# Optimization experiments

Measured on AMD Instinct MI355X. Metric: run time of the kernel, lower is better.

Reference implementation:

```python
import jax, jax.numpy as jnp
import numpy as np

# model constants (match init_kwargs)
D_EQUI = 64
D_INV = 256
D_INV_COND = 256
D_MSG = 64
N_HEADS = 16
D_FF = 256
D_EDGE_IN = 64
D_EDGE_OUT = 64
D_OUT = D_EQUI + N_HEADS + D_EDGE_OUT  # 144
IN_FEATS = 2 * D_MSG + D_EQUI + D_EDGE_IN  # 256
NEG = -1e9

B, N, NC = 2, 256, 512


def setup_inputs() -> dict:
    key = jax.random.key(0)
    ks = jax.random.split(key, 20)
    s = 0.02
    inp = {
        'equis': jax.random.normal(ks[0], (B, N, 3, D_EQUI), jnp.float32),
        'invs': jax.random.normal(ks[1], (B, N, D_INV), jnp.float32),
        'cond_equis': jax.random.normal(ks[2], (B, NC, 3, D_EQUI), jnp.float32),
        'cond_invs': jax.random.normal(ks[3], (B, NC, D_INV_COND), jnp.float32),
        'edges': jax.random.normal(ks[4], (B, N, NC, D_EDGE_IN), jnp.float32),
        'adj_matrix': jax.random.randint(ks[5], (B, N, NC), 0, 2, jnp.int32),
        # pairwise message params
        'q_w': s * jax.random.normal(ks[6], (D_INV, D_MSG), jnp.float32),
        'q_b': jnp.zeros((D_MSG,), jnp.float32),
        'k_w': s * jax.random.normal(ks[7], (D_INV_COND, D_MSG), jnp.float32),
        'k_b': jnp.zeros((D_MSG,), jnp.float32),
        'w1': s * jax.random.normal(ks[8], (IN_FEATS, D_FF), jnp.float32),
        'b1': jnp.zeros((D_FF,), jnp.float32),
        'w2': s * jax.random.normal(ks[9], (D_FF, D_OUT), jnp.float32),
        'b2': jnp.zeros((D_OUT,), jnp.float32),
        # equi attention params (bias-free linears)
        'equi_in_w': s * jax.random.normal(ks[10], (D_EQUI, D_EQUI), jnp.float32),
        'equi_out_w': s * jax.random.normal(ks[11], (D_EQUI, D_EQUI), jnp.float32),
        # inv attention params
        'inv_in_w': s * jax.random.normal(ks[12], (D_INV_COND, D_INV_COND), jnp.float32),
        'inv_in_b': jnp.zeros((D_INV_COND,), jnp.float32),
        'inv_out_w': s * jax.random.normal(ks[13], (D_INV_COND, D_INV), jnp.float32),
        'inv_out_b': jnp.zeros((D_INV,), jnp.float32),
    }
    return inp


def reference(equis, invs, cond_equis, cond_invs, edges, adj_matrix,
              q_w, q_b, k_w, k_b, w1, b1, w2, b2,
              equi_in_w, equi_out_w, inv_in_w, inv_in_b, inv_out_w, inv_out_b):
    # adjacency -> additive attention mask [B,N,NC]
    mask = jnp.where(adj_matrix > 0, 0.0, NEG).astype(equis.dtype)

    # ---- pairwise messages ----
    # per-channel dot products over the coordinate axis: [B,N,NC,D_EQUI]
    dot = jnp.einsum('bqxd,bkxd->bqkd', equis, cond_equis)
    q_msg = invs @ q_w + q_b            # [B,N,D_MSG]
    k_msg = cond_invs @ k_w + k_b       # [B,NC,D_MSG]
    feats = jnp.concatenate([
        jnp.broadcast_to(q_msg[:, :, None, :], (B, N, NC, D_MSG)),
        jnp.broadcast_to(k_msg[:, None, :, :], (B, N, NC, D_MSG)),
        dot,
        edges,
    ], axis=-1)                          # [B,N,NC,IN_FEATS]
    h = jax.nn.silu(feats @ w1 + b1)
    messages = h @ w2 + b2               # [B,N,NC,D_OUT]

    equi_m = messages[..., :D_EQUI]
    inv_m = messages[..., D_EQUI:D_EQUI + N_HEADS]
    edge_out = messages[..., D_EQUI + N_HEADS:]

    # ---- equivariant attention ----
    proj = jnp.einsum('bkxd,de->bkxe', cond_equis, equi_in_w)  # [B,NC,3,D_EQUI]
    attn_e = jax.nn.softmax(equi_m + mask[..., None], axis=2)   # [B,N,NC,D_EQUI]
    eo = jnp.einsum('bqkd,bkxd->bqxd', attn_e, proj)            # [B,N,3,D_EQUI]
    w_e = jnp.sqrt(jnp.sum(attn_e ** 2, axis=2))                # [B,N,D_EQUI]
    eo = eo * w_e[:, :, None, :]
    equi_out = jnp.einsum('bqxd,de->bqxe', eo, equi_out_w)

    # ---- invariant attention ----
    pf = cond_invs @ inv_in_w + inv_in_b                        # [B,NC,D_INV_COND]
    hf = pf.reshape(B, NC, N_HEADS, D_INV_COND // N_HEADS)      # [B,NC,H,dh]
    attn_i = jax.nn.softmax(inv_m + mask[..., None], axis=2)    # [B,N,NC,H]
    io = jnp.einsum('bqkh,bkhd->bqhd', attn_i, hf)              # [B,N,H,dh]
    w_i = jnp.sqrt(jnp.sum(attn_i ** 2, axis=2))                # [B,N,H]
    io = (io * w_i[..., None]).reshape(B, N, D_INV_COND)
    inv_out = io @ inv_out_w + inv_out_b                        # [B,N,D_INV]

    return equi_out, inv_out, edge_out
```

## Files before the change

kernel.cpp:

```cpp
#include <hip/hip_runtime.h>
#include <hip/hip_bf16.h>

#define DEVINL static __device__ __forceinline__

typedef __attribute__((ext_vector_type(8))) short bf16x8;
typedef __attribute__((ext_vector_type(8))) unsigned short us8;
typedef __attribute__((ext_vector_type(4))) float f32x4;
typedef __attribute__((ext_vector_type(4))) unsigned short us4;

DEVINL float siluf(float x) { return x / (1.0f + __expf(-x)); }
DEVINL unsigned short bfb(float x) { __hip_bfloat16 h = __float2bfloat16(x); return *(unsigned short*)&h; }
DEVINL float b2f(unsigned short u) { return __uint_as_float(((unsigned int)u) << 16); }

__global__ void wfrag_kernel(const float* __restrict__ w1, const float* __restrict__ w2,
                             unsigned short* __restrict__ w1f, unsigned short* __restrict__ w2f) {
  const int g = blockIdx.x, tid = threadIdx.x;
  if (g < 16) {
    #pragma unroll
    for (int e2 = 0; e2 < 16; ++e2) {
      const int flat = tid * 16 + e2;
      const int kk = flat >> 9, rem = flat & 511, ln = rem >> 3, e = rem & 7;
      const int c = g * 16 + (ln & 15);
      const int k = kk * 32 + (ln >> 4) * 8 + e;
      w1f[(size_t)g * 4096 + flat] = bfb(w1[(size_t)k * 256 + c]);
    }
  } else {
    const int t = g - 16;
    #pragma unroll
    for (int e2 = 0; e2 < 16; ++e2) {
      const int flat = tid * 16 + e2;
      const int kk = flat >> 9, rem = flat & 511, ln = rem >> 3, e = rem & 7;
      const int c = t * 16 + (ln & 15);
      const int k = kk * 32 + (ln >> 4) * 8 + e;
      w2f[(size_t)t * 4096 + flat] = bfb(w2[(size_t)k * 144 + c]);
    }
  }
}

__global__ void cet_kernel(const float* __restrict__ ce, unsigned short* __restrict__ cet) {
  const size_t i = (size_t)blockIdx.x * 192 + threadIdx.x;
  cet[i] = bfb(ce[i]);
}

__global__ void qk_kernel(const float* __restrict__ invs, const float* __restrict__ cond_invs,
                          const float* __restrict__ qw, const float* __restrict__ qb,
                          const float* __restrict__ kw, const float* __restrict__ kb2,
                          float* __restrict__ qm, float* __restrict__ km) {
  __shared__ float srow[256];
  const int r = blockIdx.x;
  const float* in; const float* w; const float* bias; float* out; int row;
  if (r < 512) { in = invs;      w = qw; bias = qb;  out = qm; row = r; }
  else         { in = cond_invs; w = kw; bias = kb2; out = km; row = r - 512; }
  for (int k = threadIdx.x; k < 256; k += 64) srow[k] = in[(size_t)row * 256 + k];
  __syncthreads();
  const int c = threadIdx.x;
  float acc = bias[c];
  for (int k = 0; k < 256; ++k) acc += srow[k] * w[(size_t)k * 64 + c];
  out[(size_t)row * 64 + c] = acc;
}

__global__ void projt_kernel(const float* __restrict__ ce, const float* __restrict__ eiw,
                             float* __restrict__ projt) {
  __shared__ float srow[64];
  const int r = blockIdx.x;
  const int b = r / 1536, rr = r % 1536, kn = rr / 3, x = rr % 3;
  srow[threadIdx.x] = ce[(size_t)r * 64 + threadIdx.x];
  __syncthreads();
  const int c = threadIdx.x;
  float acc = 0.f;
  for (int k = 0; k < 64; ++k) acc += srow[k] * eiw[(size_t)k * 64 + c];
  projt[((size_t)(b * 3 + x) * 64 + c) * 512 + kn] = acc;
}

__global__ void pft_kernel(const float* __restrict__ ci, const float* __restrict__ iiw,
                           const float* __restrict__ iib, float* __restrict__ pft) {
  __shared__ float srow[256];
  const int r = blockIdx.x, b = r >> 9, kn = r & 511;
  srow[threadIdx.x] = ci[(size_t)r * 256 + threadIdx.x];
  __syncthreads();
  const int c = threadIdx.x;
  float acc = iib[c];
  for (int k = 0; k < 256; ++k) acc += srow[k] * iiw[(size_t)k * 256 + c];
  pft[((size_t)(b * 256) + c) * 512 + kn] = acc;
}

__global__ __launch_bounds__(256, 2) void msg_kernel(
    const float* __restrict__ equis, const float* __restrict__ edges,
    const float* __restrict__ qm, const float* __restrict__ km,
    const unsigned short* __restrict__ cet,
    const unsigned short* __restrict__ w1f, const float* __restrict__ b1,
    const unsigned short* __restrict__ w2f, const float* __restrict__ b2,
    float* __restrict__ edge_out, __hip_bfloat16* __restrict__ sct) {
  __shared__ __align__(16) unsigned char smem[59392];
  unsigned short (*tile)[200]   = (unsigned short (*)[200])smem;
  unsigned short (*hbuf)[264]   = (unsigned short (*)[264])(smem + 25600);
  unsigned short (*ce_s)[200]   = (unsigned short (*)[200])(smem + 25600);
  unsigned short (*score_s)[88] = (unsigned short (*)[88])smem;
  float (*edge_s)[68]           = (float (*)[68])(smem + 25600);

  const int bq = blockIdx.x >> 3;
  const int b  = bq >> 8;
  const int k0 = (blockIdx.x & 7) * 64;
  const int tid = threadIdx.x;
  const int lane = tid & 63, wn = tid >> 6;
  const int lj  = lane & 15;
  const int lkb = (lane >> 4) * 8;
  const int lr4 = (lane >> 4) * 4;

  bf16x8 qf[2];
  {
    const float* qmr = qm + (size_t)bq * 64;
    #pragma unroll
    for (int kk = 0; kk < 2; ++kk) {
      const float4 a = *(const float4*)&qmr[kk * 32 + (lane >> 4) * 8];
      const float4 c = *(const float4*)&qmr[kk * 32 + (lane >> 4) * 8 + 4];
      bf16x8 v;
      v[0] = (short)bfb(a.x); v[1] = (short)bfb(a.y); v[2] = (short)bfb(a.z); v[3] = (short)bfb(a.w);
      v[4] = (short)bfb(c.x); v[5] = (short)bfb(c.y); v[6] = (short)bfb(c.z); v[7] = (short)bfb(c.w);
      qf[kk] = v;
    }
  }

  #pragma unroll
  for (int it = 0; it < 4; ++it) {
    const int flat = it * 256 + tid, row = flat >> 4, seg = flat & 15;
    const float4 v = *(const float4*)&km[((size_t)(b * 512 + k0 + row)) * 64 + seg * 4];
    us4 u = { bfb(v.x), bfb(v.y), bfb(v.z), bfb(v.w) };
    *(us4*)&tile[row][seg * 4] = u;
  }
  #pragma unroll
  for (int it = 0; it < 4; ++it) {
    const int flat = it * 256 + tid, row = flat >> 4, seg = flat & 15;
    const float4 v = *(const float4*)&edges[((size_t)bq * 512 + k0 + row) * 64 + seg * 4];
    us4 u = { bfb(v.x), bfb(v.y), bfb(v.z), bfb(v.w) };
    *(us4*)&tile[row][128 + seg * 4] = u;
  }
  #pragma unroll
  for (int it = 0; it < 6; ++it) {
    const int flat = it * 256 + tid, row = flat / 24, seg = flat % 24;
    const us8 v = *(const us8*)&cet[((size_t)(b * 512 + k0 + row)) * 192 + seg * 8];
    *(us8*)&ce_s[row][seg * 8] = v;
  }
  __syncthreads();

  {
    const int dd = tid & 63, rg = tid >> 6;
    const float e0 = equis[(size_t)bq * 192 + dd];
    const float e1 = equis[(size_t)bq * 192 + 64 + dd];
    const float e2 = equis[(size_t)bq * 192 + 128 + dd];
    #pragma unroll
    for (int it = 0; it < 16; ++it) {
      const int r = it * 4 + rg;
      const float v = e0 * b2f(ce_s[r][dd]) + e1 * b2f(ce_s[r][64 + dd]) + e2 * b2f(ce_s[r][128 + dd]);
      tile[r][64 + dd] = bfb(v);
    }
  }
  __syncthreads();

#define LW1(BUF, KK) { \
    _Pragma("unroll") for (int ct = 0; ct < 4; ++ct) \
      BUF[ct] = *(const bf16x8*)&w1f[((size_t)(((wn * 4 + ct) * 8 + (KK)) * 64) + lane) * 8]; }

#define G1STEP(KK, CUR, NXT, DOPF) { \
    if (DOPF) { LW1(NXT, (KK) + 1); } \
    if ((KK) < 2) { \
      _Pragma("unroll") for (int ct = 0; ct < 4; ++ct) \
        _Pragma("unroll") for (int rt = 0; rt < 4; ++rt) \
          acc[ct][rt] = __builtin_amdgcn_mfma_f32_16x16x32_bf16(CUR[ct], qf[KK], acc[ct][rt], 0, 0, 0); \
    } else { \
      bf16x8 fbv[4]; \
      _Pragma("unroll") for (int rt = 0; rt < 4; ++rt) \
        fbv[rt] = *(const bf16x8*)&tile[rt * 16 + lj][((KK) - 2) * 32 + lkb]; \
      _Pragma("unroll") for (int ct = 0; ct < 4; ++ct) \
        _Pragma("unroll") for (int rt = 0; rt < 4; ++rt) \
          acc[ct][rt] = __builtin_amdgcn_mfma_f32_16x16x32_bf16(CUR[ct], fbv[rt], acc[ct][rt], 0, 0, 0); \
    } }

  f32x4 acc[4][4];
  #pragma unroll
  for (int ct = 0; ct < 4; ++ct) {
    const float4 bb = *(const float4*)&b1[wn * 64 + ct * 16 + lr4];
    #pragma unroll
    for (int rt = 0; rt < 4; ++rt) { acc[ct][rt][0] = bb.x; acc[ct][rt][1] = bb.y; acc[ct][rt][2] = bb.z; acc[ct][rt][3] = bb.w; }
  }
  {
    bf16x8 waA[4], waB[4];
    LW1(waA, 0);
    G1STEP(0, waA, waB, 1)
    G1STEP(1, waB, waA, 1)
    G1STEP(2, waA, waB, 1)
    G1STEP(3, waB, waA, 1)
    G1STEP(4, waA, waB, 1)
    G1STEP(5, waB, waA, 1)
    G1STEP(6, waA, waB, 1)
    G1STEP(7, waB, waA, 0)
  }

  #pragma unroll
  for (int ct = 0; ct < 4; ++ct)
    #pragma unroll
    for (int rt = 0; rt < 4; ++rt) {
      us4 u = { bfb(siluf(acc[ct][rt][0])), bfb(siluf(acc[ct][rt][1])),
                bfb(siluf(acc[ct][rt][2])), bfb(siluf(acc[ct][rt][3])) };
      *(us4*)&hbuf[rt * 16 + lj][wn * 64 + ct * 16 + lr4] = u;
    }
  __syncthreads();

#define LW2(BUF, KK) { \
    _Pragma("unroll") for (int it = 0; it < 3; ++it) { \
      const int t = it * 4 + wn; \
      if (t < 9) BUF[it] = *(const bf16x8*)&w2f[((size_t)((t * 8 + (KK)) * 64) + lane) * 8]; } }

#define G2STEP(KK, CUR, NXT, DOPF) { \
    if (DOPF) { LW2(NXT, (KK) + 1); } \
    bf16x8 fbv[4]; \
    _Pragma("unroll") for (int rt = 0; rt < 4; ++rt) \
      fbv[rt] = *(const bf16x8*)&hbuf[rt * 16 + lj][(KK) * 32 + lkb]; \
    _Pragma("unroll") for (int it = 0; it < 3; ++it) { \
      const int t = it * 4 + wn; \
      if (t < 9) { \
        _Pragma("unroll") for (int rt = 0; rt < 4; ++rt) \
          a2[it][rt] = __builtin_amdgcn_mfma_f32_16x16x32_bf16(CUR[it], fbv[rt], a2[it][rt], 0, 0, 0); \
      } } }

  f32x4 a2[3][4];
  #pragma unroll
  for (int it = 0; it < 3; ++it) {
    const int t = it * 4 + wn;
    if (t < 9) {
      const float4 bb = *(const float4*)&b2[t * 16 + lr4];
      #pragma unroll
      for (int rt = 0; rt < 4; ++rt) { a2[it][rt][0] = bb.x; a2[it][rt][1] = bb.y; a2[it][rt][2] = bb.z; a2[it][rt][3] = bb.w; }
    }
  }
  {
    bf16x8 wbA[3], wbB[3];
    LW2(wbA, 0);
    G2STEP(0, wbA, wbB, 1)
    G2STEP(1, wbB, wbA, 1)
    G2STEP(2, wbA, wbB, 1)
    G2STEP(3, wbB, wbA, 1)
    G2STEP(4, wbA, wbB, 1)
    G2STEP(5, wbB, wbA, 1)
    G2STEP(6, wbA, wbB, 1)
    G2STEP(7, wbB, wbA, 0)
  }
  __syncthreads();

  #pragma unroll
  for (int it = 0; it < 3; ++it) {
    const int t = it * 4 + wn;
    if (t < 9) {
      if (t < 5) {
        #pragma unroll
        for (int rt = 0; rt < 4; ++rt) {
          us4 u = { bfb(a2[it][rt][0]), bfb(a2[it][rt][1]), bfb(a2[it][rt][2]), bfb(a2[it][rt][3]) };
          *(us4*)&score_s[rt * 16 + lj][t * 16 + lr4] = u;
        }
      } else {
        #pragma unroll
        for (int rt = 0; rt < 4; ++rt) {
          float4 v; v.x = a2[it][rt][0]; v.y = a2[it][rt][1]; v.z = a2[it][rt][2]; v.w = a2[it][rt][3];
          *(float4*)&edge_s[rt * 16 + lj][(t - 5) * 16 + lr4] = v;
        }
      }
    }
  }
  __syncthreads();

  #pragma unroll
  for (int it = 0; it < 3; ++it) {
    const int idx = it * 256 + tid;
    if (idx < 640) {
      const int c = idx >> 3, s = idx & 7;
      bf16x8 v;
      #pragma unroll
      for (int j = 0; j < 8; ++j) v[j] = (short)score_s[s * 8 + j][c];
      *(bf16x8*)&sct[((size_t)bq * 80 + c) * 512 + k0 + s * 8] = v;
    }
  }
  #pragma unroll
  for (int it = 0; it < 4; ++it) {
    const int idx = it * 256 + tid;
    const int row = idx >> 4, sg = idx & 15;
    *(float4*)&edge_out[((size_t)bq * 512 + k0 + row) * 64 + sg * 4] = *(const float4*)&edge_s[row][sg * 4];
  }
#undef LW1
#undef G1STEP
#undef LW2
#undef G2STEP
}

__global__ __launch_bounds__(512) void attn_kernel(
    const __hip_bfloat16* __restrict__ sct, const int* __restrict__ adj,
    const float* __restrict__ projt, const float* __restrict__ pft,
    const float* __restrict__ eow, const float* __restrict__ iow,
    const float* __restrict__ iob, float* __restrict__ out) {
  __shared__ float eo_s[3][64];
  __shared__ float io_s[256];

  const int bq = blockIdx.x, b = bq >> 8;
  const int tid = threadIdx.x, lane = tid & 63, w = tid >> 6;
  const int kb = lane * 8;

  const int4 aj0 = *(const int4*)&adj[(size_t)bq * 512 + kb];
  const int4 aj1 = *(const int4*)&adj[(size_t)bq * 512 + kb + 4];
  const unsigned int mk = (aj0.x > 0 ? 1u : 0) | (aj0.y > 0 ? 2u : 0) | (aj0.z > 0 ? 4u : 0) | (aj0.w > 0 ? 8u : 0)
                        | (aj1.x > 0 ? 16u : 0) | (aj1.y > 0 ? 32u : 0) | (aj1.z > 0 ? 64u : 0) | (aj1.w > 0 ? 128u : 0);

  for (int dd = 0; dd < 8; ++dd) {
    const int d = w * 8 + dd;
    const bf16x8 s8 = *(const bf16x8*)&sct[((size_t)bq * 80 + d) * 512 + kb];
    float p[8], z = 0.f, s2 = 0.f;
    #pragma unroll
    for (int j = 0; j < 8; ++j) {
      const float e = ((mk >> j) & 1) ? __expf(b2f((unsigned short)s8[j])) : 0.f;
      p[j] = e; z += e; s2 += e * e;
    }
    float ax[3];
    #pragma unroll
    for (int x = 0; x < 3; ++x) {
      const float* pr = projt + ((size_t)(b * 3 + x) * 64 + d) * 512 + kb;
      const float4 w0 = *(const float4*)pr;
      const float4 w1v = *(const float4*)(pr + 4);
      ax[x] = p[0] * w0.x + p[1] * w0.y + p[2] * w0.z + p[3] * w0.w
            + p[4] * w1v.x + p[5] * w1v.y + p[6] * w1v.z + p[7] * w1v.w;
    }
    #pragma unroll
    for (int off = 32; off; off >>= 1) {
      z += __shfl_xor(z, off, 64); s2 += __shfl_xor(s2, off, 64);
      ax[0] += __shfl_xor(ax[0], off, 64); ax[1] += __shfl_xor(ax[1], off, 64); ax[2] += __shfl_xor(ax[2], off, 64);
    }
    if (lane == 0) {
      const float sc = sqrtf(s2) / (z * z);
      eo_s[0][d] = ax[0] * sc; eo_s[1][d] = ax[1] * sc; eo_s[2][d] = ax[2] * sc;
    }
  }

  #pragma unroll
  for (int hh = 0; hh < 2; ++hh) {
    const int h = w * 2 + hh;
    const bf16x8 s8 = *(const bf16x8*)&sct[((size_t)bq * 80 + 64 + h) * 512 + kb];
    float p[8], z = 0.f, s2 = 0.f;
    #pragma unroll
    for (int j = 0; j < 8; ++j) {
      const float e = ((mk >> j) & 1) ? __expf(b2f((unsigned short)s8[j])) : 0.f;
      p[j] = e; z += e; s2 += e * e;
    }
    f32x4 io[4];
    #pragma unroll
    for (int d4 = 0; d4 < 4; ++d4)
      #pragma unroll
      for (int di = 0; di < 4; ++di) {
        const float* pr = pft + ((size_t)(b * 256) + h * 16 + d4 * 4 + di) * 512 + kb;
        const float4 w0 = *(const float4*)pr;
        const float4 w1v = *(const float4*)(pr + 4);
        io[d4][di] = p[0] * w0.x + p[1] * w0.y + p[2] * w0.z + p[3] * w0.w
                   + p[4] * w1v.x + p[5] * w1v.y + p[6] * w1v.z + p[7] * w1v.w;
      }
    #pragma unroll
    for (int off = 32; off; off >>= 1) {
      z += __shfl_xor(z, off, 64); s2 += __shfl_xor(s2, off, 64);
      #pragma unroll
      for (int d4 = 0; d4 < 4; ++d4)
        #pragma unroll
        for (int di = 0; di < 4; ++di)
          io[d4][di] += __shfl_xor(io[d4][di], off, 64);
    }
    if (lane == 0) {
      const float sc = sqrtf(s2) / (z * z);
      #pragma unroll
      for (int d4 = 0; d4 < 4; ++d4) {
        float4 vv; vv.x = io[d4][0] * sc; vv.y = io[d4][1] * sc; vv.z = io[d4][2] * sc; vv.w = io[d4][3] * sc;
        *(float4*)&io_s[h * 16 + d4 * 4] = vv;
      }
    }
  }
  __syncthreads();

  if (tid < 192) {
    const int x = tid >> 6, e = tid & 63;
    float a = 0.f;
    for (int d = 0; d < 64; ++d) a += eo_s[x][d] * eow[(size_t)d * 64 + e];
    out[(size_t)bq * 192 + x * 64 + e] = a;
  }
  if (tid < 256) {
    float a = iob[tid];
    for (int k = 0; k < 256; ++k) a += io_s[k] * iow[(size_t)k * 256 + tid];
    out[98304 + (size_t)bq * 256 + tid] = a;
  }
}

extern "C" void kernel_launch(void* const* d_in, const int* in_sizes, int n_in,
                              void* d_out, int out_size, void* d_ws, size_t ws_size,
                              hipStream_t stream) {
  const float* equis      = (const float*)d_in[0];
  const float* invs       = (const float*)d_in[1];
  const float* cond_equis = (const float*)d_in[2];
  const float* cond_invs  = (const float*)d_in[3];
  const float* edges      = (const float*)d_in[4];
  const int*   adj        = (const int*)d_in[5];
  const float* q_w  = (const float*)d_in[6];
  const float* q_b  = (const float*)d_in[7];
  const float* k_w  = (const float*)d_in[8];
  const float* k_b  = (const float*)d_in[9];
  const float* w1   = (const float*)d_in[10];
  const float* b1   = (const float*)d_in[11];
  const float* w2   = (const float*)d_in[12];
  const float* b2   = (const float*)d_in[13];
  const float* equi_in_w  = (const float*)d_in[14];
  const float* equi_out_w = (const float*)d_in[15];
  const float* inv_in_w   = (const float*)d_in[16];
  const float* inv_in_b   = (const float*)d_in[17];
  const float* inv_out_w  = (const float*)d_in[18];
  const float* inv_out_b  = (const float*)d_in[19];

  float* out = (float*)d_out;
  float* ws  = (float*)d_ws;
  unsigned short* w1f = (unsigned short*)ws;
  unsigned short* w2f = w1f + 65536;
  float* qm    = ws + 51200;
  float* km    = qm + 32768;
  float* projt = km + 65536;
  float* pft   = projt + 196608;
  unsigned short* cet = (unsigned short*)(pft + 262144);
  __hip_bfloat16* sct = (__hip_bfloat16*)(pft + 262144 + 98304);

  wfrag_kernel<<<25, 256, 0, stream>>>(w1, w2, w1f, w2f);
  cet_kernel<<<1024, 192, 0, stream>>>(cond_equis, cet);
  qk_kernel<<<1536, 64, 0, stream>>>(invs, cond_invs, q_w, q_b, k_w, k_b, qm, km);
  projt_kernel<<<3072, 64, 0, stream>>>(cond_equis, equi_in_w, projt);
  pft_kernel<<<1024, 256, 0, stream>>>(cond_invs, inv_in_w, inv_in_b, pft);

  msg_kernel<<<4096, 256, 0, stream>>>(equis, edges, qm, km, cet,
                                       w1f, b1, w2f, b2,
                                       out + 229376 , sct);

  attn_kernel<<<512, 512, 0, stream>>>(sct, adj, projt, pft,
                                       equi_out_w, inv_out_w, inv_out_b, out);
}
```

Baseline: 177.3 us.

## Loop msg kernel over four key tiles per block with smaller shared memory

```diff
diff --git a/kernel.cpp b/kernel.cpp
--- a/kernel.cpp
+++ b/kernel.cpp
@@ -35,11 +35,6 @@
       w2f[(size_t)t * 4096 + flat] = bfb(w2[(size_t)k * 144 + c]);
     }
   }
-}
-
-__global__ void cet_kernel(const float* __restrict__ ce, unsigned short* __restrict__ cet) {
-  const size_t i = (size_t)blockIdx.x * 192 + threadIdx.x;
-  cet[i] = bfb(ce[i]);
 }
 
 __global__ void qk_kernel(const float* __restrict__ invs, const float* __restrict__ cond_invs,
@@ -84,28 +79,28 @@
   pft[((size_t)(b * 256) + c) * 512 + kn] = acc;
 }
 
-__global__ __launch_bounds__(256, 2) void msg_kernel(
-    const float* __restrict__ equis, const float* __restrict__ edges,
+__global__ __launch_bounds__(256, 4) void msg_kernel(
+    const float* __restrict__ equis, const float* __restrict__ cond_equis,
+    const float* __restrict__ edges,
     const float* __restrict__ qm, const float* __restrict__ km,
-    const unsigned short* __restrict__ cet,
     const unsigned short* __restrict__ w1f, const float* __restrict__ b1,
     const unsigned short* __restrict__ w2f, const float* __restrict__ b2,
     float* __restrict__ edge_out, __hip_bfloat16* __restrict__ sct) {
-  __shared__ __align__(16) unsigned char smem[59392];
-  unsigned short (*tile)[200]   = (unsigned short (*)[200])smem;
-  unsigned short (*hbuf)[264]   = (unsigned short (*)[264])(smem + 25600);
-  unsigned short (*ce_s)[200]   = (unsigned short (*)[200])(smem + 25600);
-  unsigned short (*score_s)[88] = (unsigned short (*)[88])smem;
-  float (*edge_s)[68]           = (float (*)[68])(smem + 25600);
-
-  const int bq = blockIdx.x >> 3;
+  __shared__ __align__(16) unsigned short buf[64][264];
+  __shared__ float eq_s[192];
+  unsigned short (*score_s)[92] = (unsigned short (*)[92])&buf[0][0];
+  float (*edge_s)[68]           = (float (*)[68])((char*)&buf[0][0] + 11776);
+
+  const int bq = blockIdx.x >> 1;
   const int b  = bq >> 8;
-  const int k0 = (blockIdx.x & 7) * 64;
+  const int kh = blockIdx.x & 1;
   const int tid = threadIdx.x;
   const int lane = tid & 63, wn = tid >> 6;
   const int lj  = lane & 15;
   const int lkb = (lane >> 4) * 8;
   const int lr4 = (lane >> 4) * 4;
+
+  if (tid < 192) eq_s[tid] = equis[(size_t)bq * 192 + tid];
 
   bf16x8 qf[2];
   {
@@ -121,40 +116,16 @@
     }
   }
 
+  float4 bb1[4];
   #pragma unroll
-  for (int it = 0; it < 4; ++it) {
-    const int flat = it * 256 + tid, row = flat >> 4, seg = flat & 15;
-    const float4 v = *(const float4*)&km[((size_t)(b * 512 + k0 + row)) * 64 + seg * 4];
-    us4 u = { bfb(v.x), bfb(v.y), bfb(v.z), bfb(v.w) };
-    *(us4*)&tile[row][seg * 4] = u;
-  }
+  for (int ct = 0; ct < 4; ++ct) bb1[ct] = *(const float4*)&b1[wn * 64 + ct * 16 + lr4];
+  float4 bb2[3];
   #pragma unroll
-  for (int it = 0; it < 4; ++it) {
-    const int flat = it * 256 + tid, row = flat >> 4, seg = flat & 15;
-    const float4 v = *(const float4*)&edges[((size_t)bq * 512 + k0 + row) * 64 + seg * 4];
-    us4 u = { bfb(v.x), bfb(v.y), bfb(v.z), bfb(v.w) };
-    *(us4*)&tile[row][128 + seg * 4] = u;
-  }
-  #pragma unroll
-  for (int it = 0; it < 6; ++it) {
-    const int flat = it * 256 + tid, row = flat / 24, seg = flat % 24;
-    const us8 v = *(const us8*)&cet[((size_t)(b * 512 + k0 + row)) * 192 + seg * 8];
-    *(us8*)&ce_s[row][seg * 8] = v;
-  }
-  __syncthreads();
-
-  {
-    const int dd = tid & 63, rg = tid >> 6;
-    const float e0 = equis[(size_t)bq * 192 + dd];
-    const float e1 = equis[(size_t)bq * 192 + 64 + dd];
-    const float e2 = equis[(size_t)bq * 192 + 128 + dd];
-    #pragma unroll
-    for (int it = 0; it < 16; ++it) {
-      const int r = it * 4 + rg;
-      const float v = e0 * b2f(ce_s[r][dd]) + e1 * b2f(ce_s[r][64 + dd]) + e2 * b2f(ce_s[r][128 + dd]);
-      tile[r][64 + dd] = bfb(v);
-    }
-  }
+  for (int it = 0; it < 3; ++it) {
+    const int t = it * 4 + wn;
+    if (t < 9) bb2[it] = *(const float4*)&b2[t * 16 + lr4];
+  }
+
   __syncthreads();
 
 #define LW1(BUF, KK) { \
@@ -170,42 +141,12 @@
     } else { \
       bf16x8 fbv[4]; \
       _Pragma("unroll") for (int rt = 0; rt < 4; ++rt) \
-        fbv[rt] = *(const bf16x8*)&tile[rt * 16 + lj][((KK) - 2) * 32 + lkb]; \
+        fbv[rt] = *(const bf16x8*)&buf[rt * 16 + lj][((KK) - 2) * 32 + lkb]; \
       _Pragma("unroll") for (int ct = 0; ct < 4; ++ct) \
         _Pragma("unroll") for (int rt = 0; rt < 4; ++rt) \
           acc[ct][rt] = __builtin_amdgcn_mfma_f32_16x16x32_bf16(CUR[ct], fbv[rt], acc[ct][rt], 0, 0, 0); \
     } }
 
-  f32x4 acc[4][4];
-  #pragma unroll
-  for (int ct = 0; ct < 4; ++ct) {
-    const float4 bb = *(const float4*)&b1[wn * 64 + ct * 16 + lr4];
-    #pragma unroll
-    for (int rt = 0; rt < 4; ++rt) { acc[ct][rt][0] = bb.x; acc[ct][rt][1] = bb.y; acc[ct][rt][2] = bb.z; acc[ct][rt][3] = bb.w; }
-  }
-  {
-    bf16x8 waA[4], waB[4];
-    LW1(waA, 0);
-    G1STEP(0, waA, waB, 1)
-    G1STEP(1, waB, waA, 1)
-    G1STEP(2, waA, waB, 1)
-    G1STEP(3, waB, waA, 1)
-    G1STEP(4, waA, waB, 1)
-    G1STEP(5, waB, waA, 1)
-    G1STEP(6, waA, waB, 1)
-    G1STEP(7, waB, waA, 0)
-  }
-
-  #pragma unroll
-  for (int ct = 0; ct < 4; ++ct)
-    #pragma unroll
-    for (int rt = 0; rt < 4; ++rt) {
-      us4 u = { bfb(siluf(acc[ct][rt][0])), bfb(siluf(acc[ct][rt][1])),
-                bfb(siluf(acc[ct][rt][2])), bfb(siluf(acc[ct][rt][3])) };
-      *(us4*)&hbuf[rt * 16 + lj][wn * 64 + ct * 16 + lr4] = u;
-    }
-  __syncthreads();
-
 #define LW2(BUF, KK) { \
     _Pragma("unroll") for (int it = 0; it < 3; ++it) { \
       const int t = it * 4 + wn; \
@@ -215,7 +156,7 @@
     if (DOPF) { LW2(NXT, (KK) + 1); } \
     bf16x8 fbv[4]; \
     _Pragma("unroll") for (int rt = 0; rt < 4; ++rt) \
-      fbv[rt] = *(const bf16x8*)&hbuf[rt * 16 + lj][(KK) * 32 + lkb]; \
+      fbv[rt] = *(const bf16x8*)&buf[rt * 16 + lj][(KK) * 32 + lkb]; \
     _Pragma("unroll") for (int it = 0; it < 3; ++it) { \
       const int t = it * 4 + wn; \
       if (t < 9) { \
@@ -223,67 +164,146 @@
           a2[it][rt] = __builtin_amdgcn_mfma_f32_16x16x32_bf16(CUR[it], fbv[rt], a2[it][rt], 0, 0, 0); \
       } } }
 
-  f32x4 a2[3][4];
-  #pragma unroll
-  for (int it = 0; it < 3; ++it) {
-    const int t = it * 4 + wn;
-    if (t < 9) {
-      const float4 bb = *(const float4*)&b2[t * 16 + lr4];
-      #pragma unroll
-      for (int rt = 0; rt < 4; ++rt) { a2[it][rt][0] = bb.x; a2[it][rt][1] = bb.y; a2[it][rt][2] = bb.z; a2[it][rt][3] = bb.w; }
-    }
-  }
-  {
-    bf16x8 wbA[3], wbB[3];
-    LW2(wbA, 0);
-    G2STEP(0, wbA, wbB, 1)
-    G2STEP(1, wbB, wbA, 1)
-    G2STEP(2, wbA, wbB, 1)
-    G2STEP(3, wbB, wbA, 1)
-    G2STEP(4, wbA, wbB, 1)
-    G2STEP(5, wbB, wbA, 1)
-    G2STEP(6, wbA, wbB, 1)
-    G2STEP(7, wbB, wbA, 0)
-  }
-  __syncthreads();
-
-  #pragma unroll
-  for (int it = 0; it < 3; ++it) {
-    const int t = it * 4 + wn;
-    if (t < 9) {
-      if (t < 5) {
+  for (int kt = 0; kt < 4; ++kt) {
+    const int k0 = (kh * 4 + kt) * 64;
+
+    #pragma unroll
+    for (int it = 0; it < 4; ++it) {
+      const int flat = it * 256 + tid, row = flat >> 4, seg = flat & 15;
+      const float4 v = *(const float4*)&km[((size_t)(b * 512 + k0 + row)) * 64 + seg * 4];
+      us4 u = { bfb(v.x), bfb(v.y), bfb(v.z), bfb(v.w) };
+      *(us4*)&buf[row][seg * 4] = u;
+    }
+    #pragma unroll
+    for (int it = 0; it < 4; ++it) {
+      const int flat = it * 256 + tid, row = flat >> 4, seg = flat & 15;
+      const float4 v = *(const float4*)&edges[((size_t)bq * 512 + k0 + row) * 64 + seg * 4];
+      us4 u = { bfb(v.x), bfb(v.y), bfb(v.z), bfb(v.w) };
+      *(us4*)&buf[row][128 + seg * 4] = u;
+    }
+    {
+      const int r = tid >> 2, dseg = tid & 3;
+      const float* cer = cond_equis + ((size_t)(b * 512 + k0 + r)) * 192 + dseg * 16;
+      float dv[16];
+      #pragma unroll
+      for (int j = 0; j < 16; ++j) dv[j] = 0.f;
+      #pragma unroll
+      for (int sec = 0; sec < 3; ++sec) {
+        #pragma unroll
+        for (int q4 = 0; q4 < 4; ++q4) {
+          const float4 cv = *(const float4*)&cer[sec * 64 + q4 * 4];
+          const float4 ev = *(const float4*)&eq_s[sec * 64 + dseg * 16 + q4 * 4];
+          dv[q4 * 4 + 0] += cv.x * ev.x;
+          dv[q4 * 4 + 1] += cv.y * ev.y;
+          dv[q4 * 4 + 2] += cv.z * ev.z;
+          dv[q4 * 4 + 3] += cv.w * ev.w;
+        }
+      }
+      us8 o0, o1;
+      #pragma unroll
+      for (int j = 0; j < 8; ++j) { o0[j] = bfb(dv[j]); o1[j] = bfb(dv[8 + j]); }
+      *(us8*)&buf[r][64 + dseg * 16] = o0;
+      *(us8*)&buf[r][64 + dseg * 16 + 8] = o1;
+    }
+    __syncthreads();
+
+    f32x4 acc[4][4];
+    #pragma unroll
+    for (int ct = 0; ct < 4; ++ct)
+      #pragma unroll
+      for (int rt = 0; rt < 4; ++rt) {
+        acc[ct][rt][0] = bb1[ct].x; acc[ct][rt][1] = bb1[ct].y;
+        acc[ct][rt][2] = bb1[ct].z; acc[ct][rt][3] = bb1[ct].w;
+      }
+    {
+      bf16x8 waA[4], waB[4];
+      LW1(waA, 0);
+      G1STEP(0, waA, waB, 1)
+      G1STEP(1, waB, waA, 1)
+      G1STEP(2, waA, waB, 1)
+      G1STEP(3, waB, waA, 1)
+      G1STEP(4, waA, waB, 1)
+      G1STEP(5, waB, waA, 1)
+      G1STEP(6, waA, waB, 1)
+      G1STEP(7, waB, waA, 0)
+    }
+    __syncthreads();
+
+    #pragma unroll
+    for (int ct = 0; ct < 4; ++ct)
+      #pragma unroll
+      for (int rt = 0; rt < 4; ++rt) {
+        us4 u = { bfb(siluf(acc[ct][rt][0])), bfb(siluf(acc[ct][rt][1])),
+                  bfb(siluf(acc[ct][rt][2])), bfb(siluf(acc[ct][rt][3])) };
+        *(us4*)&buf[rt * 16 + lj][wn * 64 + ct * 16 + lr4] = u;
+      }
+    __syncthreads();
+
+    f32x4 a2[3][4];
+    #pragma unroll
+    for (int it = 0; it < 3; ++it) {
+      const int t = it * 4 + wn;
+      if (t < 9) {
         #pragma unroll
         for (int rt = 0; rt < 4; ++rt) {
-          us4 u = { bfb(a2[it][rt][0]), bfb(a2[it][rt][1]), bfb(a2[it][rt][2]), bfb(a2[it][rt][3]) };
-          *(us4*)&score_s[rt * 16 + lj][t * 16 + lr4] = u;
+          a2[it][rt][0] = bb2[it].x; a2[it][rt][1] = bb2[it].y;
+          a2[it][rt][2] = bb2[it].z; a2[it][rt][3] = bb2[it].w;
         }
-      } else {
+      }
+    }
+    {
+      bf16x8 wbA[3], wbB[3];
+      LW2(wbA, 0);
+      G2STEP(0, wbA, wbB, 1)
+      G2STEP(1, wbB, wbA, 1)
+      G2STEP(2, wbA, wbB, 1)
+      G2STEP(3, wbB, wbA, 1)
+      G2STEP(4, wbA, wbB, 1)
+      G2STEP(5, wbB, wbA, 1)
+      G2STEP(6, wbA, wbB, 1)
+      G2STEP(7, wbB, wbA, 0)
+    }
+    __syncthreads();
+
+    #pragma unroll
+    for (int it = 0; it < 3; ++it) {
+      const int t = it * 4 + wn;
+      if (t < 9) {
+        if (t < 5) {
+          #pragma unroll
+          for (int rt = 0; rt < 4; ++rt) {
+            us4 u = { bfb(a2[it][rt][0]), bfb(a2[it][rt][1]), bfb(a2[it][rt][2]), bfb(a2[it][rt][3]) };
+            *(us4*)&score_s[rt * 16 + lj][t * 16 + lr4] = u;
+          }
+        } else {
+          #pragma unroll
+          for (int rt = 0; rt < 4; ++rt) {
+            float4 v; v.x = a2[it][rt][0]; v.y = a2[it][rt][1]; v.z = a2[it][rt][2]; v.w = a2[it][rt][3];
+            *(float4*)&edge_s[rt * 16 + lj][(t - 5) * 16 + lr4] = v;
+          }
+        }
+      }
+    }
+    __syncthreads();
+
+    #pragma unroll
+    for (int it = 0; it < 3; ++it) {
+      const int idx = it * 256 + tid;
+      if (idx < 640) {
+        const int c = idx >> 3, s = idx & 7;
+        bf16x8 v;
         #pragma unroll
-        for (int rt = 0; rt < 4; ++rt) {
-          float4 v; v.x = a2[it][rt][0]; v.y = a2[it][rt][1]; v.z = a2[it][rt][2]; v.w = a2[it][rt][3];
-          *(float4*)&edge_s[rt * 16 + lj][(t - 5) * 16 + lr4] = v;
-        }
-      }
-    }
-  }
-  __syncthreads();
-
-  #pragma unroll
-  for (int it = 0; it < 3; ++it) {
-    const int idx = it * 256 + tid;
-    if (idx < 640) {
-      const int c = idx >> 3, s = idx & 7;
-      bf16x8 v;
-      #pragma unroll
-      for (int j = 0; j < 8; ++j) v[j] = (short)score_s[s * 8 + j][c];
-      *(bf16x8*)&sct[((size_t)bq * 80 + c) * 512 + k0 + s * 8] = v;
-    }
-  }
-  #pragma unroll
-  for (int it = 0; it < 4; ++it) {
-    const int idx = it * 256 + tid;
-    const int row = idx >> 4, sg = idx & 15;
-    *(float4*)&edge_out[((size_t)bq * 512 + k0 + row) * 64 + sg * 4] = *(const float4*)&edge_s[row][sg * 4];
+        for (int j = 0; j < 8; ++j) v[j] = (short)score_s[s * 8 + j][c];
+        *(bf16x8*)&sct[((size_t)bq * 80 + c) * 512 + k0 + s * 8] = v;
+      }
+    }
+    #pragma unroll
+    for (int it = 0; it < 4; ++it) {
+      const int idx = it * 256 + tid;
+      const int row = idx >> 4, sg = idx & 15;
+      *(float4*)&edge_out[((size_t)bq * 512 + k0 + row) * 64 + sg * 4] = *(const float4*)&edge_s[row][sg * 4];
+    }
+    __syncthreads();
   }
 #undef LW1
 #undef G1STEP
@@ -423,16 +443,14 @@
   float* km    = qm + 32768;
   float* projt = km + 65536;
   float* pft   = projt + 196608;
-  unsigned short* cet = (unsigned short*)(pft + 262144);
-  __hip_bfloat16* sct = (__hip_bfloat16*)(pft + 262144 + 98304);
+  __hip_bfloat16* sct = (__hip_bfloat16*)(pft + 262144);
 
   wfrag_kernel<<<25, 256, 0, stream>>>(w1, w2, w1f, w2f);
-  cet_kernel<<<1024, 192, 0, stream>>>(cond_equis, cet);
   qk_kernel<<<1536, 64, 0, stream>>>(invs, cond_invs, q_w, q_b, k_w, k_b, qm, km);
   projt_kernel<<<3072, 64, 0, stream>>>(cond_equis, equi_in_w, projt);
   pft_kernel<<<1024, 256, 0, stream>>>(cond_invs, inv_in_w, inv_in_b, pft);
 
-  msg_kernel<<<4096, 256, 0, stream>>>(equis, edges, qm, km, cet,
+  msg_kernel<<<1024, 256, 0, stream>>>(equis, cond_equis, edges, qm, km,
                                        w1f, b1, w2f, b2,
                                        out + 229376 , sct);
 
```

Result: slower. 546.9 us (+208.4%).
